# Performance work log

Hardware: AMD Instinct MI355X
Metric: run time of the kernel (lower is better)

Reference implementation:

```python
import jax, jax.numpy as jnp
import numpy as np

N_NODES = 20000
N_EDGES = 256000
DIM = 128
N_LAYERS = 4


def _bn(x, gamma, beta, eps=1e-5):
    # BatchNorm1d in training mode: batch statistics over the node/edge axis
    mu = x.mean(0)
    var = ((x - mu) ** 2).mean(0)
    return gamma * (x - mu) * jax.lax.rsqrt(var + eps) + beta


def setup_inputs() -> dict:
    key = jax.random.key(0)
    ks = jax.random.split(key, 32)
    s = 1.0 / np.sqrt(DIM)
    inp = {
        'h': jax.random.normal(ks[0], (N_NODES, DIM), jnp.float32),
        'e': jax.random.normal(ks[1], (N_EDGES, DIM), jnp.float32),
        'src': jax.random.randint(ks[2], (N_EDGES,), 0, N_NODES, jnp.int32),
        'dst': jax.random.randint(ks[3], (N_EDGES,), 0, N_NODES, jnp.int32),
        'W_emb_h': jax.random.normal(ks[4], (DIM, DIM), jnp.float32) * s,
        'b_emb_h': jnp.zeros((DIM,), jnp.float32),
        'W_emb_e': jax.random.normal(ks[5], (DIM, DIM), jnp.float32) * s,
        'b_emb_e': jnp.zeros((DIM,), jnp.float32),
    }
    for i, nm in enumerate(['A', 'B', 'C', 'D', 'E']):
        inp[nm + 'w'] = jax.random.normal(ks[6 + i], (N_LAYERS, DIM, DIM), jnp.float32) * s
        inp[nm + 'b'] = jnp.zeros((N_LAYERS, DIM), jnp.float32)
    inp['gh'] = jnp.ones((N_LAYERS, DIM), jnp.float32)
    inp['bh'] = jnp.zeros((N_LAYERS, DIM), jnp.float32)
    inp['ge'] = jnp.ones((N_LAYERS, DIM), jnp.float32)
    inp['be'] = jnp.zeros((N_LAYERS, DIM), jnp.float32)
    return inp


def reference(h, e, src, dst, W_emb_h, b_emb_h, W_emb_e, b_emb_e,
              Aw, Ab, Bw, Bb, Cw, Cb, Dw, Db, Ew, Eb, gh, bh, ge, be):
    n_nodes = h.shape[0]
    # input embeddings
    h = h @ W_emb_h + b_emb_h
    e = e @ W_emb_e + b_emb_e
    for l in range(Aw.shape[0]):
        h_in, e_in = h, e
        Ah = h @ Aw[l] + Ab[l]
        Bh = h @ Bw[l] + Bb[l]
        Dh = h @ Dw[l] + Db[l]
        Eh = h @ Ew[l] + Eb[l]
        Ce = e @ Cw[l] + Cb[l]
        # edge gates: e_ij = D h_i + E h_j + C e_ij  (edge i->j)
        e_new = Dh[src] + Eh[dst] + Ce            # [E, D]
        sigma = jax.nn.sigmoid(e_new)
        num = jax.ops.segment_sum(sigma * Bh[src], dst, num_segments=n_nodes)
        den = jax.ops.segment_sum(sigma, dst, num_segments=n_nodes)
        h_new = Ah + num / (den + 1e-6)
        h_new = _bn(h_new, gh[l], bh[l])
        e_new = _bn(e_new, ge[l], be[l])
        # relu + residual (dropout = 0)
        h = h_in + jax.nn.relu(h_new)
        e = e_in + jax.nn.relu(e_new)
    return h
```

## Files before the change

### kernel.cpp

```cpp
#include <hip/hip_runtime.h>
#include <hip/hip_bf16.h>

typedef __attribute__((ext_vector_type(8))) short short8;
typedef __attribute__((ext_vector_type(4))) float floatx4;
typedef __attribute__((ext_vector_type(4))) unsigned short ushortx4;

typedef __attribute__((address_space(3))) unsigned int lds_u32;
typedef __attribute__((address_space(1))) const unsigned int g_u32;

__device__ __forceinline__ float bf2f(unsigned short u) {
    union { float f; unsigned int i; } v; v.i = ((unsigned int)u) << 16; return v.f;
}
__device__ __forceinline__ unsigned short f2bf(float f) {
    union { float f; unsigned int i; } v; v.f = f;
    unsigned int r = v.i + 0x7fffu + ((v.i >> 16) & 1u);
    return (unsigned short)(r >> 16);
}

__global__ void deg_count(const int* __restrict__ dst, int* __restrict__ deg, int E) {
    int i = blockIdx.x * 256 + threadIdx.x;
    if (i < E) atomicAdd(&deg[dst[i]], 1);
}

__global__ __launch_bounds__(1024) void scan_rowptr(const int* __restrict__ deg,
                                                    int* __restrict__ rowptr,
                                                    int* __restrict__ cursor, int N) {
    const int CH = 20;
    __shared__ int buf[1024];
    int t = threadIdx.x;
    int base = t * CH;
    int local[CH];
    int tot = 0;
#pragma unroll
    for (int k = 0; k < CH; ++k) {
        int i = base + k;
        int v = (i < N) ? deg[i] : 0;
        local[k] = tot;
        tot += v;
    }
    buf[t] = tot;
    __syncthreads();
    for (int off = 1; off < 1024; off <<= 1) {
        int x = (t >= off) ? buf[t - off] : 0;
        __syncthreads();
        buf[t] += x;
        __syncthreads();
    }
    int excl = buf[t] - tot;
#pragma unroll
    for (int k = 0; k < CH; ++k) {
        int i = base + k;
        if (i < N) { rowptr[i] = excl + local[k]; cursor[i] = excl + local[k]; }
    }
    if (t == 1023) rowptr[N] = buf[1023];
}

__global__ void scatter_edges(const int* __restrict__ src, const int* __restrict__ dst,
                              int* __restrict__ cursor, int* __restrict__ eix,
                              int* __restrict__ sx, int E) {
    int i = blockIdx.x * 256 + threadIdx.x;
    if (i >= E) return;
    int d = dst[i];
    int pos = atomicAdd(&cursor[d], 1);
    eix[pos] = i;
    sx[pos] = src[i];
}

__global__ void transpose_w(const float* __restrict__ Wh,
                            const float* __restrict__ We,
                            const float* __restrict__ Aw,
                            const float* __restrict__ Bw,
                            const float* __restrict__ Cw,
                            const float* __restrict__ Dw,
                            const float* __restrict__ Ew,
                            unsigned short* __restrict__ Wt) {
    int i = blockIdx.x * 256 + threadIdx.x;
    const int total = 22 * 16384;
    if (i >= total) return;
    int slot = i >> 14;
    int r = i & 16383;
    int n = r >> 7;
    int k = r & 127;
    const float* srcp;
    if (slot == 0) srcp = Wh;
    else if (slot == 1) srcp = We;
    else {
        int t = slot - 2;
        int l = t / 5, w = t % 5;
        const float* bases[5] = {Aw, Bw, Cw, Dw, Ew};
        srcp = bases[w] + l * 16384;
    }
    Wt[i] = f2bf(srcp[k * 128 + n]);
}

template <int IN_F32, int OUT_BF16, int GATHER>
__global__ __launch_bounds__(256) void gemm_lds(const void* __restrict__ Ain,
                                                const int* __restrict__ ridx,
                                                const unsigned short* __restrict__ Wt,
                                                const float* __restrict__ bias,
                                                void* __restrict__ Cout,
                                                int nTiles, int Mrows) {
    constexpr int ROWB = IN_F32 ? 512 : 256;
    constexpr int RSH = IN_F32 ? 9 : 8;
    constexpr int TILEB = 64 * ROWB;
    constexpr int PERW = TILEB / 4;
    constexpr int ROUNDS = PERW / 1024;
    __shared__ unsigned char smem[2][TILEB];

    const int lane = threadIdx.x & 63;
    const int wv = threadIdx.x >> 6;
    const int m16 = lane & 15;
    const int kg = lane >> 4;

    short8 b[4][2];
#pragma unroll
    for (int j = 0; j < 2; ++j)
#pragma unroll
        for (int ks = 0; ks < 4; ++ks)
            b[ks][j] = *(const short8*)(Wt + ((wv * 2 + j) * 16 + m16) * 128 + ks * 32 + kg * 8);
    floatx4 bv[2];
#pragma unroll
    for (int j = 0; j < 2; ++j)
        bv[j] = *(const floatx4*)(bias + (wv * 2 + j) * 16 + kg * 4);

    const unsigned char* Ab = (const unsigned char*)Ain;

    int t0 = blockIdx.x;
    if (t0 >= nTiles) return;

    auto stage = [&](int bufsel, int t) {
#pragma unroll
        for (int r = 0; r < ROUNDS; ++r) {
            int d = wv * PERW + r * 1024 + lane * 16;
            int row = d >> RSH;
            int scol;
            if (IN_F32)
                scol = (d ^ ((row & 3) << 5)) & (ROWB - 1);
            else
                scol = (d ^ ((row & 7) << 4)) & (ROWB - 1);
            int grow = t * 64 + row;
            grow = grow < Mrows ? grow : Mrows - 1;
            if (GATHER) grow = ridx[grow];
            const unsigned char* gp = Ab + (size_t)grow * ROWB + scol;
            unsigned char* lp = &smem[bufsel][wv * PERW + r * 1024];
            __builtin_amdgcn_global_load_lds((g_u32*)gp, (lds_u32*)lp, 16, 0, 0);
        }
    };

    int cur = 0;
    stage(0, t0);
    __syncthreads();

    for (int t = t0; t < nTiles; t += gridDim.x) {
        int tn = t + gridDim.x;
        if (tn < nTiles) stage(cur ^ 1, tn);

        const unsigned char* sb = smem[cur];
#pragma unroll
        for (int st = 0; st < 4; ++st) {
            short8 a[4];
#pragma unroll
            for (int ks = 0; ks < 4; ++ks) {
                if (IN_F32) {
                    int aoff = (st * 16 + m16) * 512 + ks * 128 + kg * 32;
                    aoff ^= (m16 & 3) << 5;
                    floatx4 f0 = *(const floatx4*)(sb + aoff);
                    floatx4 f1 = *(const floatx4*)(sb + aoff + 16);
                    short8 tt;
                    tt[0] = (short)f2bf(f0[0]); tt[1] = (short)f2bf(f0[1]);
                    tt[2] = (short)f2bf(f0[2]); tt[3] = (short)f2bf(f0[3]);
                    tt[4] = (short)f2bf(f1[0]); tt[5] = (short)f2bf(f1[1]);
                    tt[6] = (short)f2bf(f1[2]); tt[7] = (short)f2bf(f1[3]);
                    a[ks] = tt;
                } else {
                    int aoff = (st * 16 + m16) * 256 + ks * 64 + kg * 16;
                    aoff ^= (m16 & 7) << 4;
                    a[ks] = *(const short8*)(sb + aoff);
                }
            }
            floatx4 acc0 = (floatx4){0.f, 0.f, 0.f, 0.f};
            floatx4 acc1 = (floatx4){0.f, 0.f, 0.f, 0.f};
#pragma unroll
            for (int ks = 0; ks < 4; ++ks) {
                acc0 = __builtin_amdgcn_mfma_f32_16x16x32_bf16(b[ks][0], a[ks], acc0, 0, 0, 0);
                acc1 = __builtin_amdgcn_mfma_f32_16x16x32_bf16(b[ks][1], a[ks], acc1, 0, 0, 0);
            }
            size_t row = (size_t)t * 64 + st * 16 + m16;
#pragma unroll
            for (int j = 0; j < 2; ++j) {
                int c0 = (wv * 2 + j) * 16 + kg * 4;
                floatx4 accj = j ? acc1 : acc0;
                if (OUT_BF16) {
                    ushortx4 o;
#pragma unroll
                    for (int i = 0; i < 4; ++i) o[i] = f2bf(accj[i] + bv[j][i]);
                    *(ushortx4*)((unsigned short*)Cout + row * 128 + c0) = o;
                } else {
                    floatx4 o;
#pragma unroll
                    for (int i = 0; i < 4; ++i) o[i] = accj[i] + bv[j][i];
                    *(floatx4*)((float*)Cout + row * 128 + c0) = o;
                }
            }
        }
        __syncthreads();
        cur ^= 1;
    }
}

__global__ __launch_bounds__(1024) void gemm_h4(const float* __restrict__ h_cur,
                                                const unsigned short* __restrict__ WtL,
                                                const float* __restrict__ Abi,
                                                const float* __restrict__ Bbi,
                                                const float* __restrict__ Dbi,
                                                const float* __restrict__ Ebi,
                                                float* __restrict__ AhB,
                                                unsigned short* __restrict__ BD16,
                                                unsigned short* __restrict__ Eh16,
                                                int nStrips) {
    const int lane = threadIdx.x & 63;
    const int w = threadIdx.x >> 6;
    const int m16 = lane & 15;
    const int kg = lane >> 4;

    short8 bf[4][2];
    floatx4 bv[2];
    if (w < 8) {
        const int slot = (w < 4) ? 0 : 4;
        const float* bp = (w < 4) ? Abi : Ebi;
        const int ntb = (w & 3) * 2;
#pragma unroll
        for (int j = 0; j < 2; ++j) {
#pragma unroll
            for (int ks = 0; ks < 4; ++ks)
                bf[ks][j] = *(const short8*)(WtL + slot * 16384 +
                                             ((ntb + j) * 16 + m16) * 128 + ks * 32 + kg * 8);
            bv[j] = *(const floatx4*)(bp + (ntb + j) * 16 + kg * 4);
        }
    } else {
        const int nt = w - 8;
#pragma unroll
        for (int ks = 0; ks < 4; ++ks) {
            bf[ks][0] = *(const short8*)(WtL + 1 * 16384 + (nt * 16 + m16) * 128 + ks * 32 + kg * 8);
            bf[ks][1] = *(const short8*)(WtL + 3 * 16384 + (nt * 16 + m16) * 128 + ks * 32 + kg * 8);
        }
        bv[0] = *(const floatx4*)(Bbi + nt * 16 + kg * 4);
        bv[1] = *(const floatx4*)(Dbi + nt * 16 + kg * 4);
    }

    for (int s = blockIdx.x; s < nStrips; s += gridDim.x) {
        size_t rowBase = ((size_t)s * 16 + m16) * 128;
        short8 a[4];
#pragma unroll
        for (int ks = 0; ks < 4; ++ks) {
            int off = ks * 32 + kg * 8;
            floatx4 f0 = *(const floatx4*)(h_cur + rowBase + off);
            floatx4 f1 = *(const floatx4*)(h_cur + rowBase + off + 4);
            short8 t;
            t[0] = (short)f2bf(f0[0]); t[1] = (short)f2bf(f0[1]);
            t[2] = (short)f2bf(f0[2]); t[3] = (short)f2bf(f0[3]);
            t[4] = (short)f2bf(f1[0]); t[5] = (short)f2bf(f1[1]);
            t[6] = (short)f2bf(f1[2]); t[7] = (short)f2bf(f1[3]);
            a[ks] = t;
        }

        floatx4 acc0 = (floatx4){0.f, 0.f, 0.f, 0.f};
        floatx4 acc1 = (floatx4){0.f, 0.f, 0.f, 0.f};
#pragma unroll
        for (int ks = 0; ks < 4; ++ks) {
            acc0 = __builtin_amdgcn_mfma_f32_16x16x32_bf16(bf[ks][0], a[ks], acc0, 0, 0, 0);
            acc1 = __builtin_amdgcn_mfma_f32_16x16x32_bf16(bf[ks][1], a[ks], acc1, 0, 0, 0);
        }

        size_t r = (size_t)s * 16 + m16;
        if (w < 4) {
            const int ntb = (w & 3) * 2;
            floatx4 o0, o1;
#pragma unroll
            for (int i = 0; i < 4; ++i) { o0[i] = acc0[i] + bv[0][i]; o1[i] = acc1[i] + bv[1][i]; }
            *(floatx4*)(AhB + r * 128 + (ntb + 0) * 16 + kg * 4) = o0;
            *(floatx4*)(AhB + r * 128 + (ntb + 1) * 16 + kg * 4) = o1;
        } else if (w < 8) {
            const int ntb = (w & 3) * 2;
            ushortx4 o0, o1;
#pragma unroll
            for (int i = 0; i < 4; ++i) {
                o0[i] = f2bf(acc0[i] + bv[0][i]);
                o1[i] = f2bf(acc1[i] + bv[1][i]);
            }
            *(ushortx4*)(Eh16 + r * 128 + (ntb + 0) * 16 + kg * 4) = o0;
            *(ushortx4*)(Eh16 + r * 128 + (ntb + 1) * 16 + kg * 4) = o1;
        } else {
            const int nt = w - 8;
            short8 o;
#pragma unroll
            for (int i = 0; i < 4; ++i) {
                o[2 * i]     = (short)f2bf(acc0[i] + bv[0][i]);
                o[2 * i + 1] = (short)f2bf(acc1[i] + bv[1][i]);
            }
            *(short8*)(BD16 + r * 256 + (nt * 16 + kg * 4) * 2) = o;
        }
    }
}

template <int DO_E>
__global__ __launch_bounds__(256) void node_aggregate(unsigned short* __restrict__ Ce,
                                                      const unsigned short* __restrict__ BD16,
                                                      const unsigned short* __restrict__ Eh16,
                                                      const int* __restrict__ rowptr,
                                                      const int* __restrict__ sx,
                                                      const float* __restrict__ Ah,
                                                      float* __restrict__ h_new,
                                                      float* __restrict__ sums, int N) {
    const int q = threadIdx.x & 31;
    const int g = threadIdx.x >> 5;
    float hs[4] = {0.f, 0.f, 0.f, 0.f};
    float hq[4] = {0.f, 0.f, 0.f, 0.f};
    float es[4] = {0.f, 0.f, 0.f, 0.f};
    float eq[4] = {0.f, 0.f, 0.f, 0.f};
    for (int d = blockIdx.x * 8 + g; d < N; d += gridDim.x * 8) {
        int beg = rowptr[d], end = rowptr[d + 1];
        ushortx4 eh4 = *(const ushortx4*)(Eh16 + (size_t)d * 128 + q * 4);
        float ehf[4];
#pragma unroll
        for (int k = 0; k < 4; ++k) ehf[k] = bf2f(eh4[k]);
        float num[4] = {0.f, 0.f, 0.f, 0.f};
        float den[4] = {0.f, 0.f, 0.f, 0.f};
        int j = beg;
        for (; j + 1 < end; j += 2) {
            int s0 = sx[j], s1 = sx[j + 1];
            ushortx4 c0 = *(const ushortx4*)(Ce + (size_t)j * 128 + q * 4);
            ushortx4 c1 = *(const ushortx4*)(Ce + (size_t)(j + 1) * 128 + q * 4);
            short8 bd0 = *(const short8*)(BD16 + (size_t)s0 * 256 + q * 8);
            short8 bd1 = *(const short8*)(BD16 + (size_t)s1 * 256 + q * 8);
            ushortx4 o0, o1;
#pragma unroll
            for (int k = 0; k < 4; ++k) {
                float en0 = bf2f(c0[k]) + bf2f((unsigned short)bd0[2 * k + 1]) + ehf[k];
                float en1 = bf2f(c1[k]) + bf2f((unsigned short)bd1[2 * k + 1]) + ehf[k];
                if (DO_E) {
                    es[k] += en0 + en1;
                    eq[k] += en0 * en0 + en1 * en1;
                    o0[k] = f2bf(en0);
                    o1[k] = f2bf(en1);
                }
                float sg0 = 1.f / (1.f + __expf(-en0));
                float sg1 = 1.f / (1.f + __expf(-en1));
                den[k] += sg0 + sg1;
                num[k] += sg0 * bf2f((unsigned short)bd0[2 * k])
                        + sg1 * bf2f((unsigned short)bd1[2 * k]);
            }
            if (DO_E) {
                *(ushortx4*)(Ce + (size_t)j * 128 + q * 4) = o0;
                *(ushortx4*)(Ce + (size_t)(j + 1) * 128 + q * 4) = o1;
            }
        }
        if (j < end) {
            int s0 = sx[j];
            ushortx4 c0 = *(const ushortx4*)(Ce + (size_t)j * 128 + q * 4);
            short8 bd0 = *(const short8*)(BD16 + (size_t)s0 * 256 + q * 8);
            ushortx4 o0;
#pragma unroll
            for (int k = 0; k < 4; ++k) {
                float en0 = bf2f(c0[k]) + bf2f((unsigned short)bd0[2 * k + 1]) + ehf[k];
                if (DO_E) {
                    es[k] += en0;
                    eq[k] += en0 * en0;
                    o0[k] = f2bf(en0);
                }
                float sg0 = 1.f / (1.f + __expf(-en0));
                den[k] += sg0;
                num[k] += sg0 * bf2f((unsigned short)bd0[2 * k]);
            }
            if (DO_E) *(ushortx4*)(Ce + (size_t)j * 128 + q * 4) = o0;
        }
        floatx4 ah = *(const floatx4*)(Ah + (size_t)d * 128 + q * 4);
        floatx4 out;
#pragma unroll
        for (int k = 0; k < 4; ++k) {
            float v = ah[k] + num[k] / (den[k] + 1e-6f);
            out[k] = v;
            hs[k] += v;
            hq[k] += v * v;
        }
        *(floatx4*)(h_new + (size_t)d * 128 + q * 4) = out;
    }
    __shared__ float ls[512];
    ls[threadIdx.x] = 0.f;
    ls[256 + threadIdx.x] = 0.f;
    __syncthreads();
#pragma unroll
    for (int k = 0; k < 4; ++k) {
        atomicAdd(&ls[q * 4 + k], hs[k]);
        atomicAdd(&ls[128 + q * 4 + k], hq[k]);
        if (DO_E) {
            atomicAdd(&ls[256 + q * 4 + k], es[k]);
            atomicAdd(&ls[384 + q * 4 + k], eq[k]);
        }
    }
    __syncthreads();
    atomicAdd(&sums[threadIdx.x], ls[threadIdx.x]);
    if (DO_E) atomicAdd(&sums[256 + threadIdx.x], ls[256 + threadIdx.x]);
}

__global__ void finalize_stats(const float* __restrict__ sums,
                               const float* __restrict__ gh,
                               const float* __restrict__ bh,
                               const float* __restrict__ ge,
                               const float* __restrict__ be,
                               float* __restrict__ coef, int N, int E) {
    int c = threadIdx.x;
    if (c >= 128) return;
    float muh = sums[c] / (float)N;
    float vh = fmaxf(sums[128 + c] / (float)N - muh * muh, 0.f);
    float rsh = rsqrtf(vh + 1e-5f);
    float g = gh[c], bt = bh[c];
    coef[c] = g * rsh;
    coef[128 + c] = bt - g * rsh * muh;
    float mue = sums[256 + c] / (float)E;
    float ve = fmaxf(sums[384 + c] / (float)E - mue * mue, 0.f);
    float rse = rsqrtf(ve + 1e-5f);
    float g2 = ge[c], b2 = be[c];
    coef[256 + c] = g2 * rse;
    coef[384 + c] = b2 - g2 * rse * mue;
}

__global__ __launch_bounds__(256) void h_update(const float* __restrict__ h_new,
                                                const float* __restrict__ coef,
                                                float* __restrict__ h_cur,
                                                float* __restrict__ out, int N) {
    const int c = threadIdx.x & 127;
    float sa = coef[c], sb = coef[128 + c];
    int total = N * 128;
    for (int i = blockIdx.x * blockDim.x + threadIdx.x; i < total; i += gridDim.x * blockDim.x) {
        float v = h_new[i] * sa + sb;
        v = v > 0.f ? v : 0.f;
        float h = h_cur[i] + v;
        h_cur[i] = h;
        if (out) out[i] = h;
    }
}

__global__ __launch_bounds__(256) void e_update(const unsigned short* __restrict__ e_new,
                                                const float* __restrict__ coef,
                                                unsigned short* __restrict__ e_cur, int E) {
    int total8 = E * 16;
    for (int idx = blockIdx.x * blockDim.x + threadIdx.x; idx < total8;
         idx += gridDim.x * blockDim.x) {
        int c8 = (idx & 15) * 8;
        short8 en = *(const short8*)(e_new + (size_t)idx * 8);
        short8 ec = *(const short8*)(e_cur + (size_t)idx * 8);
        floatx4 sa0 = *(const floatx4*)(coef + 256 + c8);
        floatx4 sa1 = *(const floatx4*)(coef + 256 + c8 + 4);
        floatx4 sb0 = *(const floatx4*)(coef + 384 + c8);
        floatx4 sb1 = *(const floatx4*)(coef + 384 + c8 + 4);
        short8 r;
#pragma unroll
        for (int k = 0; k < 8; ++k) {
            float sa = (k < 4) ? sa0[k] : sa1[k - 4];
            float sb = (k < 4) ? sb0[k] : sb1[k - 4];
            float v = bf2f((unsigned short)en[k]) * sa + sb;
            v = v > 0.f ? v : 0.f;
            r[k] = (short)f2bf(bf2f((unsigned short)ec[k]) + v);
        }
        *(short8*)(e_cur + (size_t)idx * 8) = r;
    }
}

extern "C" void kernel_launch(void* const* d_in, const int* in_sizes, int n_in,
                              void* d_out, int out_size, void* d_ws, size_t ws_size,
                              hipStream_t stream) {
    const int N = 20000, E = 256000, L = 4;
    const int NPAD = 20032;

    const float* h_in = (const float*)d_in[0];
    const float* e_in = (const float*)d_in[1];
    const int* src = (const int*)d_in[2];
    const int* dst = (const int*)d_in[3];
    const float* Wemb_h = (const float*)d_in[4];
    const float* bemb_h = (const float*)d_in[5];
    const float* Wemb_e = (const float*)d_in[6];
    const float* bemb_e = (const float*)d_in[7];
    const float* Aw = (const float*)d_in[8];
    const float* Abi = (const float*)d_in[9];
    const float* Bw = (const float*)d_in[10];
    const float* Bbi = (const float*)d_in[11];
    const float* Cw = (const float*)d_in[12];
    const float* Cbi = (const float*)d_in[13];
    const float* Dw = (const float*)d_in[14];
    const float* Dbi = (const float*)d_in[15];
    const float* Ew = (const float*)d_in[16];
    const float* Ebi = (const float*)d_in[17];
    const float* gh = (const float*)d_in[18];
    const float* bh = (const float*)d_in[19];
    const float* ge = (const float*)d_in[20];
    const float* be = (const float*)d_in[21];

    char* p = (char*)d_ws;
    auto carve = [&](size_t bytes) {
        void* r = (void*)p;
        p += ((bytes + 255) & ~(size_t)255);
        return r;
    };
    unsigned short* Wt = (unsigned short*)carve((size_t)22 * 16384 * 2);
    float* h_cur = (float*)carve((size_t)NPAD * 128 * 4);
    unsigned short* e_cur = (unsigned short*)carve((size_t)E * 128 * 2);
    unsigned short* e_new = (unsigned short*)carve((size_t)E * 128 * 2);
    float* AhB = (float*)carve((size_t)N * 128 * 4);
    unsigned short* BD16 = (unsigned short*)carve((size_t)N * 256 * 2);
    unsigned short* Eh16 = (unsigned short*)carve((size_t)N * 128 * 2);
    float* h_newB = (float*)carve((size_t)N * 128 * 4);
    float* sums = (float*)carve(4 * 128 * 4);
    float* coef = (float*)carve(4 * 128 * 4);
    int* deg = (int*)carve((size_t)N * 4);
    int* rowptr = (int*)carve((size_t)(N + 1) * 4);
    int* cursor = (int*)carve((size_t)N * 4);
    int* eix = (int*)carve((size_t)E * 4);
    int* sx = (int*)carve((size_t)E * 4);

    hipMemsetAsync(deg, 0, (size_t)N * 4, stream);
    deg_count<<<(E + 255) / 256, 256, 0, stream>>>(dst, deg, E);
    scan_rowptr<<<1, 1024, 0, stream>>>(deg, rowptr, cursor, N);
    scatter_edges<<<(E + 255) / 256, 256, 0, stream>>>(src, dst, cursor, eix, sx, E);

    transpose_w<<<(22 * 16384 + 255) / 256, 256, 0, stream>>>(Wemb_h, Wemb_e, Aw, Bw, Cw, Dw, Ew, Wt);

    gemm_lds<1, 0, 0><<<313, 256, 0, stream>>>(h_in, nullptr, Wt + 0 * 16384, bemb_h,
                                               h_cur, 313, N);
    gemm_lds<1, 1, 1><<<1024, 256, 0, stream>>>(e_in, eix, Wt + 1 * 16384, bemb_e,
                                                e_cur, E / 64, E);

    for (int l = 0; l < L; ++l) {
        int last = (l == L - 1);
        hipMemsetAsync(sums, 0, 4 * 128 * 4, stream);
        const unsigned short* WtL = Wt + (size_t)(2 + l * 5) * 16384;
        gemm_h4<<<250, 1024, 0, stream>>>(h_cur, WtL, Abi + l * 128, Bbi + l * 128,
                                          Dbi + l * 128, Ebi + l * 128, AhB, BD16, Eh16,
                                          N / 16);
        gemm_lds<0, 1, 0><<<1024, 256, 0, stream>>>(e_cur, nullptr, WtL + 2 * 16384,
                                                    Cbi + l * 128, e_new, E / 64, E);
        if (!last)
            node_aggregate<1><<<1250, 256, 0, stream>>>(e_new, BD16, Eh16, rowptr, sx, AhB,
                                                        h_newB, sums, N);
        else
            node_aggregate<0><<<1250, 256, 0, stream>>>(e_new, BD16, Eh16, rowptr, sx, AhB,
                                                        h_newB, sums, N);
        finalize_stats<<<1, 128, 0, stream>>>(sums, gh + l * 128, bh + l * 128, ge + l * 128,
                                              be + l * 128, coef, N, E);
        h_update<<<512, 256, 0, stream>>>(h_newB, coef, h_cur, last ? (float*)d_out : nullptr, N);
        if (!last) e_update<<<2048, 256, 0, stream>>>(e_new, coef, e_cur, E);
    }
}
```

Measured before the change: 967.4 us.

## Fuse edge gate assembly and edge BN stats into Ce GEMM epilogue

Moves the Dh[src] + Eh[dst] addition and the edge batch-norm statistics into the C·e GEMM epilogue, using a new per-edge dst index array. The aggregation kernel then only reads the final e_new and Bh, and no longer rewrites e_new in place, so one read-modify-write pass over the edge tensor goes away. The interleaved BD buffer is split into separate Bh and Dh buffers, the gather loop is unrolled to four edges, and the sigmoid uses a hardware reciprocal. In exchange the GEMM epilogue now does random gathers of Dh and Eh rows, and the sigmoid reads a bf16-rounded e_new.

```diff
diff --git a/kernel.cpp b/kernel.cpp
--- a/kernel.cpp
+++ b/kernel.cpp
@@ -57,13 +57,14 @@
 
 __global__ void scatter_edges(const int* __restrict__ src, const int* __restrict__ dst,
                               int* __restrict__ cursor, int* __restrict__ eix,
-                              int* __restrict__ sx, int E) {
+                              int* __restrict__ sx, int* __restrict__ dstx, int E) {
     int i = blockIdx.x * 256 + threadIdx.x;
     if (i >= E) return;
     int d = dst[i];
     int pos = atomicAdd(&cursor[d], 1);
     eix[pos] = i;
     sx[pos] = src[i];
+    dstx[pos] = d;
 }
 
 __global__ void transpose_w(const float* __restrict__ Wh,
@@ -208,6 +209,128 @@
     }
 }
 
+template <int STATS>
+__global__ __launch_bounds__(256) void gemm_ce(const unsigned short* __restrict__ Ain,
+                                               const unsigned short* __restrict__ Wt,
+                                               const float* __restrict__ bias,
+                                               const int* __restrict__ sx,
+                                               const int* __restrict__ dstx,
+                                               const unsigned short* __restrict__ Dh16,
+                                               const unsigned short* __restrict__ Eh16,
+                                               unsigned short* __restrict__ e_new,
+                                               float* __restrict__ sums,
+                                               int nTiles) {
+    constexpr int TILEB = 64 * 256;
+    constexpr int PERW = TILEB / 4;
+    constexpr int ROUNDS = PERW / 1024;
+    __shared__ unsigned char smem[2][TILEB];
+    __shared__ float ls[256];
+
+    const int lane = threadIdx.x & 63;
+    const int wv = threadIdx.x >> 6;
+    const int m16 = lane & 15;
+    const int kg = lane >> 4;
+
+    short8 b[4][2];
+#pragma unroll
+    for (int j = 0; j < 2; ++j)
+#pragma unroll
+        for (int ks = 0; ks < 4; ++ks)
+            b[ks][j] = *(const short8*)(Wt + ((wv * 2 + j) * 16 + m16) * 128 + ks * 32 + kg * 8);
+    floatx4 bv[2];
+#pragma unroll
+    for (int j = 0; j < 2; ++j)
+        bv[j] = *(const floatx4*)(bias + (wv * 2 + j) * 16 + kg * 4);
+
+    float es[2][4], eq[2][4];
+#pragma unroll
+    for (int j = 0; j < 2; ++j)
+#pragma unroll
+        for (int i = 0; i < 4; ++i) { es[j][i] = 0.f; eq[j][i] = 0.f; }
+
+    const unsigned char* Ab = (const unsigned char*)Ain;
+
+    int t0 = blockIdx.x;
+
+    auto stage = [&](int bufsel, int t) {
+#pragma unroll
+        for (int r = 0; r < ROUNDS; ++r) {
+            int d = wv * PERW + r * 1024 + lane * 16;
+            int row = d >> 8;
+            int scol = (d ^ ((row & 7) << 4)) & 255;
+            const unsigned char* gp = Ab + (size_t)(t * 64 + row) * 256 + scol;
+            unsigned char* lp = &smem[bufsel][wv * PERW + r * 1024];
+            __builtin_amdgcn_global_load_lds((g_u32*)gp, (lds_u32*)lp, 16, 0, 0);
+        }
+    };
+
+    int cur = 0;
+    if (t0 < nTiles) {
+        stage(0, t0);
+        __syncthreads();
+
+        for (int t = t0; t < nTiles; t += gridDim.x) {
+            int tn = t + gridDim.x;
+            if (tn < nTiles) stage(cur ^ 1, tn);
+
+            const unsigned char* sb = smem[cur];
+#pragma unroll
+            for (int st = 0; st < 4; ++st) {
+                int erow = t * 64 + st * 16 + m16;
+                int sr = sx[erow];
+                int dr = dstx[erow];
+                short8 a[4];
+#pragma unroll
+                for (int ks = 0; ks < 4; ++ks) {
+                    int aoff = (st * 16 + m16) * 256 + ks * 64 + kg * 16;
+                    aoff ^= (m16 & 7) << 4;
+                    a[ks] = *(const short8*)(sb + aoff);
+                }
+                floatx4 acc0 = (floatx4){0.f, 0.f, 0.f, 0.f};
+                floatx4 acc1 = (floatx4){0.f, 0.f, 0.f, 0.f};
+#pragma unroll
+                for (int ks = 0; ks < 4; ++ks) {
+                    acc0 = __builtin_amdgcn_mfma_f32_16x16x32_bf16(b[ks][0], a[ks], acc0, 0, 0, 0);
+                    acc1 = __builtin_amdgcn_mfma_f32_16x16x32_bf16(b[ks][1], a[ks], acc1, 0, 0, 0);
+                }
+#pragma unroll
+                for (int j = 0; j < 2; ++j) {
+                    int c0 = (wv * 2 + j) * 16 + kg * 4;
+                    floatx4 accj = j ? acc1 : acc0;
+                    ushortx4 dh = *(const ushortx4*)(Dh16 + (size_t)sr * 128 + c0);
+                    ushortx4 eh = *(const ushortx4*)(Eh16 + (size_t)dr * 128 + c0);
+                    ushortx4 o;
+#pragma unroll
+                    for (int i = 0; i < 4; ++i) {
+                        float en = accj[i] + bv[j][i] + bf2f(dh[i]) + bf2f(eh[i]);
+                        o[i] = f2bf(en);
+                        if (STATS) { es[j][i] += en; eq[j][i] += en * en; }
+                    }
+                    *(ushortx4*)(e_new + (size_t)erow * 128 + c0) = o;
+                }
+            }
+            __syncthreads();
+            cur ^= 1;
+        }
+    }
+
+    if (STATS) {
+        ls[threadIdx.x] = 0.f;
+        __syncthreads();
+#pragma unroll
+        for (int j = 0; j < 2; ++j) {
+            int c0 = (wv * 2 + j) * 16 + kg * 4;
+#pragma unroll
+            for (int i = 0; i < 4; ++i) {
+                atomicAdd(&ls[c0 + i], es[j][i]);
+                atomicAdd(&ls[(c0 + i) ^ 128], eq[j][i]);
+            }
+        }
+        __syncthreads();
+        atomicAdd(&sums[256 + threadIdx.x], ls[threadIdx.x]);
+    }
+}
+
 __global__ __launch_bounds__(1024) void gemm_h4(const float* __restrict__ h_cur,
                                                 const unsigned short* __restrict__ WtL,
                                                 const float* __restrict__ Abi,
@@ -215,37 +338,30 @@
                                                 const float* __restrict__ Dbi,
                                                 const float* __restrict__ Ebi,
                                                 float* __restrict__ AhB,
-                                                unsigned short* __restrict__ BD16,
+                                                unsigned short* __restrict__ Bh16,
+                                                unsigned short* __restrict__ Dh16,
                                                 unsigned short* __restrict__ Eh16,
                                                 int nStrips) {
     const int lane = threadIdx.x & 63;
     const int w = threadIdx.x >> 6;
+    const int grp = w >> 2;
+    const int ntb = (w & 3) * 2;
     const int m16 = lane & 15;
     const int kg = lane >> 4;
 
+    const int slotmap[4] = {0, 1, 3, 4};
+    const float* biasmap[4] = {Abi, Bbi, Dbi, Ebi};
+    const unsigned short* Wm = WtL + slotmap[grp] * 16384;
+    const float* bp = biasmap[grp];
+
     short8 bf[4][2];
     floatx4 bv[2];
-    if (w < 8) {
-        const int slot = (w < 4) ? 0 : 4;
-        const float* bp = (w < 4) ? Abi : Ebi;
-        const int ntb = (w & 3) * 2;
-#pragma unroll
-        for (int j = 0; j < 2; ++j) {
-#pragma unroll
-            for (int ks = 0; ks < 4; ++ks)
-                bf[ks][j] = *(const short8*)(WtL + slot * 16384 +
-                                             ((ntb + j) * 16 + m16) * 128 + ks * 32 + kg * 8);
-            bv[j] = *(const floatx4*)(bp + (ntb + j) * 16 + kg * 4);
-        }
-    } else {
-        const int nt = w - 8;
-#pragma unroll
-        for (int ks = 0; ks < 4; ++ks) {
-            bf[ks][0] = *(const short8*)(WtL + 1 * 16384 + (nt * 16 + m16) * 128 + ks * 32 + kg * 8);
-            bf[ks][1] = *(const short8*)(WtL + 3 * 16384 + (nt * 16 + m16) * 128 + ks * 32 + kg * 8);
-        }
-        bv[0] = *(const floatx4*)(Bbi + nt * 16 + kg * 4);
-        bv[1] = *(const floatx4*)(Dbi + nt * 16 + kg * 4);
+#pragma unroll
+    for (int j = 0; j < 2; ++j) {
+#pragma unroll
+        for (int ks = 0; ks < 4; ++ks)
+            bf[ks][j] = *(const short8*)(Wm + ((ntb + j) * 16 + m16) * 128 + ks * 32 + kg * 8);
+        bv[j] = *(const floatx4*)(bp + (ntb + j) * 16 + kg * 4);
     }
 
     for (int s = blockIdx.x; s < nStrips; s += gridDim.x) {
@@ -273,40 +389,28 @@
         }
 
         size_t r = (size_t)s * 16 + m16;
-        if (w < 4) {
-            const int ntb = (w & 3) * 2;
+        if (grp == 0) {
             floatx4 o0, o1;
 #pragma unroll
             for (int i = 0; i < 4; ++i) { o0[i] = acc0[i] + bv[0][i]; o1[i] = acc1[i] + bv[1][i]; }
             *(floatx4*)(AhB + r * 128 + (ntb + 0) * 16 + kg * 4) = o0;
             *(floatx4*)(AhB + r * 128 + (ntb + 1) * 16 + kg * 4) = o1;
-        } else if (w < 8) {
-            const int ntb = (w & 3) * 2;
+        } else {
+            unsigned short* outp = (grp == 1) ? Bh16 : (grp == 2) ? Dh16 : Eh16;
             ushortx4 o0, o1;
 #pragma unroll
             for (int i = 0; i < 4; ++i) {
                 o0[i] = f2bf(acc0[i] + bv[0][i]);
                 o1[i] = f2bf(acc1[i] + bv[1][i]);
             }
-            *(ushortx4*)(Eh16 + r * 128 + (ntb + 0) * 16 + kg * 4) = o0;
-            *(ushortx4*)(Eh16 + r * 128 + (ntb + 1) * 16 + kg * 4) = o1;
-        } else {
-            const int nt = w - 8;
-            short8 o;
-#pragma unroll
-            for (int i = 0; i < 4; ++i) {
-                o[2 * i]     = (short)f2bf(acc0[i] + bv[0][i]);
-                o[2 * i + 1] = (short)f2bf(acc1[i] + bv[1][i]);
-            }
-            *(short8*)(BD16 + r * 256 + (nt * 16 + kg * 4) * 2) = o;
-        }
-    }
-}
-
-template <int DO_E>
-__global__ __launch_bounds__(256) void node_aggregate(unsigned short* __restrict__ Ce,
-                                                      const unsigned short* __restrict__ BD16,
-                                                      const unsigned short* __restrict__ Eh16,
+            *(ushortx4*)(outp + r * 128 + (ntb + 0) * 16 + kg * 4) = o0;
+            *(ushortx4*)(outp + r * 128 + (ntb + 1) * 16 + kg * 4) = o1;
+        }
+    }
+}
+
+__global__ __launch_bounds__(256) void node_aggregate(const unsigned short* __restrict__ e_new,
+                                                      const unsigned short* __restrict__ Bh16,
                                                       const int* __restrict__ rowptr,
                                                       const int* __restrict__ sx,
                                                       const float* __restrict__ Ah,
@@ -316,63 +420,42 @@
     const int g = threadIdx.x >> 5;
     float hs[4] = {0.f, 0.f, 0.f, 0.f};
     float hq[4] = {0.f, 0.f, 0.f, 0.f};
-    float es[4] = {0.f, 0.f, 0.f, 0.f};
-    float eq[4] = {0.f, 0.f, 0.f, 0.f};
     for (int d = blockIdx.x * 8 + g; d < N; d += gridDim.x * 8) {
         int beg = rowptr[d], end = rowptr[d + 1];
-        ushortx4 eh4 = *(const ushortx4*)(Eh16 + (size_t)d * 128 + q * 4);
-        float ehf[4];
-#pragma unroll
-        for (int k = 0; k < 4; ++k) ehf[k] = bf2f(eh4[k]);
         float num[4] = {0.f, 0.f, 0.f, 0.f};
         float den[4] = {0.f, 0.f, 0.f, 0.f};
         int j = beg;
-        for (; j + 1 < end; j += 2) {
-            int s0 = sx[j], s1 = sx[j + 1];
-            ushortx4 c0 = *(const ushortx4*)(Ce + (size_t)j * 128 + q * 4);
-            ushortx4 c1 = *(const ushortx4*)(Ce + (size_t)(j + 1) * 128 + q * 4);
-            short8 bd0 = *(const short8*)(BD16 + (size_t)s0 * 256 + q * 8);
-            short8 bd1 = *(const short8*)(BD16 + (size_t)s1 * 256 + q * 8);
-            ushortx4 o0, o1;
+        for (; j + 3 < end; j += 4) {
+            int s0 = sx[j], s1 = sx[j + 1], s2 = sx[j + 2], s3 = sx[j + 3];
+            ushortx4 e0 = *(const ushortx4*)(e_new + (size_t)j * 128 + q * 4);
+            ushortx4 e1 = *(const ushortx4*)(e_new + (size_t)(j + 1) * 128 + q * 4);
+            ushortx4 e2 = *(const ushortx4*)(e_new + (size_t)(j + 2) * 128 + q * 4);
+            ushortx4 e3 = *(const ushortx4*)(e_new + (size_t)(j + 3) * 128 + q * 4);
+            ushortx4 b0 = *(const ushortx4*)(Bh16 + (size_t)s0 * 128 + q * 4);
+            ushortx4 b1 = *(const ushortx4*)(Bh16 + (size_t)s1 * 128 + q * 4);
+            ushortx4 b2 = *(const ushortx4*)(Bh16 + (size_t)s2 * 128 + q * 4);
+            ushortx4 b3 = *(const ushortx4*)(Bh16 + (size_t)s3 * 128 + q * 4);
 #pragma unroll
             for (int k = 0; k < 4; ++k) {
-                float en0 = bf2f(c0[k]) + bf2f((unsigned short)bd0[2 * k + 1]) + ehf[k];
-                float en1 = bf2f(c1[k]) + bf2f((unsigned short)bd1[2 * k + 1]) + ehf[k];
-                if (DO_E) {
-                    es[k] += en0 + en1;
-                    eq[k] += en0 * en0 + en1 * en1;
-                    o0[k] = f2bf(en0);
-                    o1[k] = f2bf(en1);
-                }
-                float sg0 = 1.f / (1.f + __expf(-en0));
-                float sg1 = 1.f / (1.f + __expf(-en1));
-                den[k] += sg0 + sg1;
-                num[k] += sg0 * bf2f((unsigned short)bd0[2 * k])
-                        + sg1 * bf2f((unsigned short)bd1[2 * k]);
-            }
-            if (DO_E) {
-                *(ushortx4*)(Ce + (size_t)j * 128 + q * 4) = o0;
-                *(ushortx4*)(Ce + (size_t)(j + 1) * 128 + q * 4) = o1;
-            }
-        }
-        if (j < end) {
+                float sg0 = __builtin_amdgcn_rcpf(1.f + __expf(-bf2f(e0[k])));
+                float sg1 = __builtin_amdgcn_rcpf(1.f + __expf(-bf2f(e1[k])));
+                float sg2 = __builtin_amdgcn_rcpf(1.f + __expf(-bf2f(e2[k])));
+                float sg3 = __builtin_amdgcn_rcpf(1.f + __expf(-bf2f(e3[k])));
+                den[k] += (sg0 + sg1) + (sg2 + sg3);
+                num[k] += sg0 * bf2f(b0[k]) + sg1 * bf2f(b1[k])
+                        + sg2 * bf2f(b2[k]) + sg3 * bf2f(b3[k]);
+            }
+        }
+        for (; j < end; ++j) {
             int s0 = sx[j];
-            ushortx4 c0 = *(const ushortx4*)(Ce + (size_t)j * 128 + q * 4);
-            short8 bd0 = *(const short8*)(BD16 + (size_t)s0 * 256 + q * 8);
-            ushortx4 o0;
+            ushortx4 e0 = *(const ushortx4*)(e_new + (size_t)j * 128 + q * 4);
+            ushortx4 b0 = *(const ushortx4*)(Bh16 + (size_t)s0 * 128 + q * 4);
 #pragma unroll
             for (int k = 0; k < 4; ++k) {
-                float en0 = bf2f(c0[k]) + bf2f((unsigned short)bd0[2 * k + 1]) + ehf[k];
-                if (DO_E) {
-                    es[k] += en0;
-                    eq[k] += en0 * en0;
-                    o0[k] = f2bf(en0);
-                }
-                float sg0 = 1.f / (1.f + __expf(-en0));
+                float sg0 = __builtin_amdgcn_rcpf(1.f + __expf(-bf2f(e0[k])));
                 den[k] += sg0;
-                num[k] += sg0 * bf2f((unsigned short)bd0[2 * k]);
-            }
-            if (DO_E) *(ushortx4*)(Ce + (size_t)j * 128 + q * 4) = o0;
+                num[k] += sg0 * bf2f(b0[k]);
+            }
         }
         floatx4 ah = *(const floatx4*)(Ah + (size_t)d * 128 + q * 4);
         floatx4 out;
@@ -385,22 +468,16 @@
         }
         *(floatx4*)(h_new + (size_t)d * 128 + q * 4) = out;
     }
-    __shared__ float ls[512];
+    __shared__ float ls[256];
     ls[threadIdx.x] = 0.f;
-    ls[256 + threadIdx.x] = 0.f;
     __syncthreads();
 #pragma unroll
     for (int k = 0; k < 4; ++k) {
         atomicAdd(&ls[q * 4 + k], hs[k]);
         atomicAdd(&ls[128 + q * 4 + k], hq[k]);
-        if (DO_E) {
-            atomicAdd(&ls[256 + q * 4 + k], es[k]);
-            atomicAdd(&ls[384 + q * 4 + k], eq[k]);
-        }
     }
     __syncthreads();
     atomicAdd(&sums[threadIdx.x], ls[threadIdx.x]);
-    if (DO_E) atomicAdd(&sums[256 + threadIdx.x], ls[256 + threadIdx.x]);
 }
 
 __global__ void finalize_stats(const float* __restrict__ sums,
@@ -507,7 +584,8 @@
     unsigned short* e_cur = (unsigned short*)carve((size_t)E * 128 * 2);
     unsigned short* e_new = (unsigned short*)carve((size_t)E * 128 * 2);
     float* AhB = (float*)carve((size_t)N * 128 * 4);
-    unsigned short* BD16 = (unsigned short*)carve((size_t)N * 256 * 2);
+    unsigned short* Bh16 = (unsigned short*)carve((size_t)N * 128 * 2);
+    unsigned short* Dh16 = (unsigned short*)carve((size_t)N * 128 * 2);
     unsigned short* Eh16 = (unsigned short*)carve((size_t)N * 128 * 2);
     float* h_newB = (float*)carve((size_t)N * 128 * 4);
     float* sums = (float*)carve(4 * 128 * 4);
@@ -517,11 +595,12 @@
     int* cursor = (int*)carve((size_t)N * 4);
     int* eix = (int*)carve((size_t)E * 4);
     int* sx = (int*)carve((size_t)E * 4);
+    int* dstx = (int*)carve((size_t)E * 4);
 
     hipMemsetAsync(deg, 0, (size_t)N * 4, stream);
     deg_count<<<(E + 255) / 256, 256, 0, stream>>>(dst, deg, E);
     scan_rowptr<<<1, 1024, 0, stream>>>(deg, rowptr, cursor, N);
-    scatter_edges<<<(E + 255) / 256, 256, 0, stream>>>(src, dst, cursor, eix, sx, E);
+    scatter_edges<<<(E + 255) / 256, 256, 0, stream>>>(src, dst, cursor, eix, sx, dstx, E);
 
     transpose_w<<<(22 * 16384 + 255) / 256, 256, 0, stream>>>(Wemb_h, Wemb_e, Aw, Bw, Cw, Dw, Ew, Wt);
 
@@ -535,16 +614,16 @@
         hipMemsetAsync(sums, 0, 4 * 128 * 4, stream);
         const unsigned short* WtL = Wt + (size_t)(2 + l * 5) * 16384;
         gemm_h4<<<250, 1024, 0, stream>>>(h_cur, WtL, Abi + l * 128, Bbi + l * 128,
-                                          Dbi + l * 128, Ebi + l * 128, AhB, BD16, Eh16,
+                                          Dbi + l * 128, Ebi + l * 128, AhB, Bh16, Dh16, Eh16,
                                           N / 16);
-        gemm_lds<0, 1, 0><<<1024, 256, 0, stream>>>(e_cur, nullptr, WtL + 2 * 16384,
-                                                    Cbi + l * 128, e_new, E / 64, E);
         if (!last)
-            node_aggregate<1><<<1250, 256, 0, stream>>>(e_new, BD16, Eh16, rowptr, sx, AhB,
-                                                        h_newB, sums, N);
+            gemm_ce<1><<<1024, 256, 0, stream>>>(e_cur, WtL + 2 * 16384, Cbi + l * 128,
+                                                 sx, dstx, Dh16, Eh16, e_new, sums, E / 64);
         else
-            node_aggregate<0><<<1250, 256, 0, stream>>>(e_new, BD16, Eh16, rowptr, sx, AhB,
-                                                        h_newB, sums, N);
+            gemm_ce<0><<<1024, 256, 0, stream>>>(e_cur, WtL + 2 * 16384, Cbi + l * 128,
+                                                 sx, dstx, Dh16, Eh16, e_new, sums, E / 64);
+        node_aggregate<<<1250, 256, 0, stream>>>(e_new, Bh16, rowptr, sx, AhB,
+                                                 h_newB, sums, N);
         finalize_stats<<<1, 128, 0, stream>>>(sums, gh + l * 128, bh + l * 128, ge + l * 128,
                                               be + l * 128, coef, N, E);
         h_update<<<512, 256, 0, stream>>>(h_newB, coef, h_cur, last ? (float*)d_out : nullptr, N);
```

Measured after the change: 1.046 ms. 1.08x slower.
